# Optimization experiments

Measured on AMD Instinct MI355X. Metric: run time of the kernel, lower is better.

The kernel has to match this reference:

```python
import jax, jax.numpy as jnp
import numpy as np

NUM_EXPERTS = 8
HIDDEN = 2048
FFN = 1376
CAPACITY_FACTOR = 1.25
SCORE_SCALE = 1.0


def setup_inputs() -> dict:
    key = jax.random.key(0)
    k = jax.random.split(key, 6)
    T = 8192
    x = jax.random.normal(k[0], (T, HIDDEN), dtype=jnp.float32)
    topK_indices = jax.random.randint(k[1], (T,), 0, NUM_EXPERTS, dtype=jnp.int64)
    topK_scores = jax.random.uniform(k[2], (T,), dtype=jnp.float32)
    s = 1.0 / np.sqrt(HIDDEN)
    w_gate = jax.random.normal(k[3], (NUM_EXPERTS, HIDDEN, FFN), dtype=jnp.float32) * s
    w_up = jax.random.normal(k[4], (NUM_EXPERTS, HIDDEN, FFN), dtype=jnp.float32) * s
    w_down = jax.random.normal(k[5], (NUM_EXPERTS, FFN, HIDDEN), dtype=jnp.float32) * (1.0 / np.sqrt(FFN))
    return {"x": x, "topK_indices": topK_indices, "topK_scores": topK_scores,
            "w_gate": w_gate, "w_up": w_up, "w_down": w_down}


def reference(x, topK_indices, topK_scores, w_gate, w_up, w_down):
    T, D = x.shape
    E = w_gate.shape[0]
    capacity = int(CAPACITY_FACTOR * T / E)  # static (depends only on shapes)
    # position of each token within its assigned expert (deterministic drop:
    # keep the first `capacity` tokens in sequence order per expert)
    oh = jax.nn.one_hot(topK_indices, E, dtype=jnp.int32)          # [T,E]
    rank = jnp.take_along_axis(jnp.cumsum(oh, axis=0) - 1,
                               topK_indices[:, None].astype(jnp.int32), axis=1)[:, 0]
    keep = rank < capacity                                          # [T]
    # dispatch into per-expert capacity buffers; dropped tokens go to dummy slot
    slot = jnp.where(keep, topK_indices.astype(jnp.int32) * capacity + rank, E * capacity)
    buf = jnp.zeros((E * capacity + 1, D), x.dtype)
    buf = buf.at[slot].set(jnp.where(keep[:, None], x, jnp.zeros_like(x)))
    xe = buf[:E * capacity].reshape(E, capacity, D)                 # [E,C,D]
    # per-expert SwiGLU MLP as grouped GEMMs
    h = jax.nn.silu(jnp.einsum('ecd,edf->ecf', xe, w_gate)) * jnp.einsum('ecd,edf->ecf', xe, w_up)
    out = jnp.einsum('ecf,efd->ecd', h, w_down).reshape(E * capacity, D)
    out = jnp.concatenate([out, jnp.zeros((1, D), out.dtype)], axis=0)
    # combine: dropped tokens -> zero (dropped_padding='zero'), gate-score fusion
    y = out[slot] * keep[:, None].astype(out.dtype)
    y = y * (topK_scores[:, None] * SCORE_SCALE)
    return y
```

## Files before the change

kernel.cpp:

```cpp
#include <hip/hip_runtime.h>
#include <hip/hip_bf16.h>
#include <cstdint>
#include <cstddef>

#define NTOK 8192
#define DH   2048
#define DF   1376
#define NE   8
#define CAP  1280

typedef __bf16 bf16x8 __attribute__((ext_vector_type(8)));
typedef float  f32x4  __attribute__((ext_vector_type(4)));

#define BARRIER() asm volatile("s_barrier" ::: "memory")
#define WAITV(n)  asm volatile("s_waitcnt vmcnt(" #n ")" ::: "memory")
#define LGKM(n)   asm volatile("s_waitcnt lgkmcnt(" #n ")" ::: "memory")
#define SCHED0()  __builtin_amdgcn_sched_barrier(0)
#define SETPRIO(n) __builtin_amdgcn_s_setprio(n)

__device__ __forceinline__ uint32_t pk2(float a, float b) {
  float2 f; f.x = a; f.y = b;
  union { __hip_bfloat162 h; uint32_t u; } cv;
  cv.h = __float22bfloat162_rn(f);
  return cv.u;
}
__device__ __forceinline__ ushort bf16bits(float a) {
  return (ushort)(pk2(a, 0.f) & 0xFFFFu);
}
__device__ __forceinline__ void gload16(const ushort* g, ushort* l) {
  __builtin_amdgcn_global_load_lds(
      (const __attribute__((address_space(1))) uint32_t*)(const void*)g,
      (__attribute__((address_space(3))) uint32_t*)(void*)l,
      16, 0, 0);
}

__device__ __forceinline__ int rp_off(int row, int l4) {
  return ((row >> 1) << 7) + (((((row & 1) << 2) + l4) ^ ((row >> 1) & 7)) << 4);
}

__global__ void routing_kernel(const int* __restrict__ idx, int* __restrict__ tok_slot,
                               int* __restrict__ tok2slot) {
  __shared__ int cnt[256][NE];
  const int t = threadIdx.x;
  for (int s = t; s < NE * CAP; s += 256) tok_slot[s] = -1;
  unsigned long long cA = 0ull, cB = 0ull;
  const int per = NTOK / 256, base = t * per;
  for (int i = 0; i < per; ++i) {
    int e = idx[base + i];
    unsigned long long inc = 1ull << ((e & 3) * 16);
    if (e < 4) cA += inc; else cB += inc;
  }
#pragma unroll
  for (int e = 0; e < 4; ++e) cnt[t][e]     = (int)((cA >> (e * 16)) & 0xFFFF);
#pragma unroll
  for (int e = 0; e < 4; ++e) cnt[t][4 + e] = (int)((cB >> (e * 16)) & 0xFFFF);
  __syncthreads();
  if (t < NE) {
    int run = 0;
    for (int i = 0; i < 256; ++i) { int c = cnt[i][t]; cnt[i][t] = run; run += c; }
  }
  __syncthreads();
  cA = 0ull; cB = 0ull;
#pragma unroll
  for (int e = 0; e < 4; ++e) cA |= (unsigned long long)(cnt[t][e] & 0xFFFF) << (e * 16);
#pragma unroll
  for (int e = 0; e < 4; ++e) cB |= (unsigned long long)(cnt[t][4 + e] & 0xFFFF) << (e * 16);
  for (int i = 0; i < per; ++i) {
    int token = base + i;
    int e = idx[token];
    int sh = (e & 3) * 16;
    int r = (int)(((e < 4 ? cA : cB) >> sh) & 0xFFFF);
    unsigned long long inc = 1ull << sh;
    if (e < 4) cA += inc; else cB += inc;
    bool keep = (r < CAP);
    tok2slot[token] = keep ? (e * CAP + r) : -1;
    if (keep) tok_slot[e * CAP + r] = token;
  }
}

__global__ __launch_bounds__(256) void prep1(
    const float* __restrict__ wg, const float* __restrict__ wu,
    ushort* __restrict__ wgt, ushort* __restrict__ wut,
    const float* __restrict__ x, const int* __restrict__ tok2slot,
    ushort* __restrict__ xb2, float* __restrict__ y) {
  const int z = blockIdx.z;
  const int tid = threadIdx.x;
  if (z >= 16) {
    const int row = (z - 16) * 1024 + blockIdx.y * 32 + blockIdx.x;
    const int k0 = tid * 8;
    const size_t off = (size_t)row * DH + k0;
    float4 a = *(const float4*)(x + off);
    float4 b = *(const float4*)(x + off + 4);
    uint4 p4 = { pk2(a.x, a.y), pk2(a.z, a.w), pk2(b.x, b.y), pk2(b.z, b.w) };
    int slotg = tok2slot[row];
    if (slotg < 0) {
      float4 zz = {0.f, 0.f, 0.f, 0.f};
      *(float4*)(y + off) = zz;
      *(float4*)(y + off + 4) = zz;
    } else {
      int e = slotg / CAP, srow = slotg - e * CAP;
      int mt = srow >> 8, r = srow & 255;
      int kt = k0 >> 5, kk = k0 & 31;
      int p = r >> 1, g = ((r & 1) << 2) + (kk >> 3);
      size_t ou = (size_t)((e * 5 + mt) * 64 + kt) * 8192 + p * 64 + ((g ^ (p & 7)) << 3);
      *(uint4*)(xb2 + ou) = p4;
    }
    return;
  }
  const float* in; ushort* out; int eidx;
  if (z < 8) { in = wg; out = wgt; eidx = z; }
  else       { in = wu; out = wut; eidx = z - 8; }
  const int K = DH, N = DF;
  const int n0 = blockIdx.x * 64, k0 = blockIdx.y * 64;
  if (n0 >= N) return;
  __shared__ ushort T[64][72];
  const size_t eoff_in = (size_t)eidx * K * N;
  const int kr = tid >> 4;
  const int nc = (tid & 15) * 4;
#pragma unroll
  for (int it = 0; it < 4; ++it) {
    int k = k0 + kr + it * 16;
    int n = n0 + nc;
    float4 v = {0.f, 0.f, 0.f, 0.f};
    if (k < K && n + 4 <= N) v = *(const float4*)(in + eoff_in + (size_t)k * N + n);
    T[nc + 0][kr + it * 16] = bf16bits(v.x);
    T[nc + 1][kr + it * 16] = bf16bits(v.y);
    T[nc + 2][kr + it * 16] = bf16bits(v.z);
    T[nc + 3][kr + it * 16] = bf16bits(v.w);
  }
  __syncthreads();
  const int nr = tid >> 2;
  const int kc = tid & 3;
#pragma unroll
  for (int it = 0; it < 2; ++it) {
    int kloc = kc * 16 + it * 8;
    int n = n0 + nr, k = k0 + kloc;
    if (n < N && k + 8 <= K) {
      int nt = n >> 7, r = n & 127;
      int kt = k >> 5, kk = k & 31;
      int p = r >> 1, g = ((r & 1) << 2) + (kk >> 3);
      size_t ou = (size_t)((eidx * 11 + nt) * 64 + kt) * 4096 + p * 64 + ((g ^ (p & 7)) << 3);
      *(uint4*)(out + ou) = *(const uint4*)&T[nr][kloc];
    }
  }
}

__global__ __launch_bounds__(256) void prep_wd(
    const float* __restrict__ wd, ushort* __restrict__ wdt) {
  const int eidx = blockIdx.z;
  const int K = DF, N = DH;
  const int n0 = blockIdx.x * 64, k0 = blockIdx.y * 64;
  __shared__ ushort T[64][72];
  const int tid = threadIdx.x;
  const size_t eoff_in = (size_t)eidx * K * N;
  const int kr = tid >> 4;
  const int nc = (tid & 15) * 4;
#pragma unroll
  for (int it = 0; it < 4; ++it) {
    int k = k0 + kr + it * 16;
    int n = n0 + nc;
    float4 v = {0.f, 0.f, 0.f, 0.f};
    if (k < K && n + 4 <= N) v = *(const float4*)(wd + eoff_in + (size_t)k * N + n);
    T[nc + 0][kr + it * 16] = bf16bits(v.x);
    T[nc + 1][kr + it * 16] = bf16bits(v.y);
    T[nc + 2][kr + it * 16] = bf16bits(v.z);
    T[nc + 3][kr + it * 16] = bf16bits(v.w);
  }
  __syncthreads();
  const int nr = tid >> 2;
  const int kc = tid & 3;
#pragma unroll
  for (int it = 0; it < 2; ++it) {
    int kloc = kc * 16 + it * 8;
    int n = n0 + nr, k = k0 + kloc;
    if (n < N && k + 8 <= K) {
      int nt = n >> 7, r = n & 127;
      int kt = k >> 5, kk = k & 31;
      int p = r >> 1, g = ((r & 1) << 2) + (kk >> 3);
      size_t ou = (size_t)((eidx * 16 + nt) * 43 + kt) * 4096 + p * 64 + ((g ^ (p & 7)) << 3);
      *(uint4*)(wdt + ou) = *(const uint4*)&T[nr][kloc];
    }
  }
}

#define GU_READ(SET, RB) { \
  char* Ab_  = sm + (RB) * 16384; \
  char* Bgb_ = sm + 65536 + (RB) * 8192; \
  char* Bub_ = sm + 98304 + (RB) * 8192; \
  _Pragma("unroll") for (int i_ = 0; i_ < 4; ++i_) aR##SET[i_]  = *(const bf16x8*)(Ab_ + aoff[i_]); \
  _Pragma("unroll") for (int j_ = 0; j_ < 4; ++j_) bgR##SET[j_] = *(const bf16x8*)(Bgb_ + boff[j_]); \
  _Pragma("unroll") for (int j_ = 0; j_ < 4; ++j_) buR##SET[j_] = *(const bf16x8*)(Bub_ + boff[j_]); \
}
#define GU_MFMA(SET) { \
  _Pragma("unroll") for (int j_ = 0; j_ < 4; ++j_) \
    _Pragma("unroll") for (int i_ = 0; i_ < 4; ++i_) \
      accG[i_][j_] = __builtin_amdgcn_mfma_f32_16x16x32_bf16(aR##SET[i_], bgR##SET[j_], accG[i_][j_], 0, 0, 0); \
  _Pragma("unroll") for (int j_ = 0; j_ < 4; ++j_) \
    _Pragma("unroll") for (int i_ = 0; i_ < 4; ++i_) \
      accU[i_][j_] = __builtin_amdgcn_mfma_f32_16x16x32_bf16(aR##SET[i_], buR##SET[j_], accU[i_][j_], 0, 0, 0); \
}
#define GU_BODY(T, CUR, NXT) { \
  const int t_ = (T); \
  if (t_ + 3 < NT) { \
    const int w_ = (t_ + 3) & 3; \
    gload16(srcA[0] + (size_t)(t_ + 3) * 8192, (ushort*)(sm + w_ * 16384 + dstw)); \
    gload16(srcA[1] + (size_t)(t_ + 3) * 8192, (ushort*)(sm + w_ * 16384 + 8192 + dstw)); \
    gload16(srcBg + (size_t)(t_ + 3) * 4096, (ushort*)(sm + 65536 + w_ * 8192 + dstw)); \
    gload16(srcBu + (size_t)(t_ + 3) * 4096, (ushort*)(sm + 98304 + w_ * 8192 + dstw)); \
  } \
  if (t_ + 1 < NT) { GU_READ(NXT, (t_ + 1) & 3); LGKM(12); } else { LGKM(0); } \
  SCHED0(); SETPRIO(1); \
  GU_MFMA(CUR); \
  SETPRIO(0); SCHED0(); \
  if (t_ + 3 < NT) { WAITV(4); } else if (t_ + 2 < NT) { WAITV(0); } \
  BARRIER(); \
}

__global__ __launch_bounds__(512, 2) void gemm_gateup3(
    const ushort* __restrict__ xb2, const ushort* __restrict__ wgt,
    const ushort* __restrict__ wut, ushort* __restrict__ h)
{
  __shared__ __align__(16) char sm[131072];
  const int tid = threadIdx.x, lane = tid & 63, wid = tid >> 6;
  const int wr = wid >> 1, wc = wid & 1;
  const int l15 = lane & 15, l4 = lane >> 4;

  int wgid = (blockIdx.x & 7) * 55 + (blockIdx.x >> 3);
  const int e = wgid / 55;
  const int rem = wgid - e * 55;
  const int mt = rem / 11, nt = rem - (rem / 11) * 11;
  const int n0 = nt * 128;

  const ushort* srcA[2]; const ushort* srcBg; const ushort* srcBu;
  {
    const size_t abase = (size_t)((e * 5 + mt) * 64) * 8192;
    const int lo = (wid * 1024 + lane * 16) >> 1;
    srcA[0] = xb2 + abase + lo;
    srcA[1] = xb2 + abase + 4096 + lo;
    const size_t bbase = (size_t)((e * 11 + nt) * 64) * 4096;
    srcBg = wgt + bbase + lo;
    srcBu = wut + bbase + lo;
  }
  int aoff[4], boff[4];
#pragma unroll
  for (int i = 0; i < 4; ++i) aoff[i] = rp_off(wr * 64 + i * 16 + l15, l4);
#pragma unroll
  for (int j = 0; j < 4; ++j) boff[j] = rp_off(wc * 64 + j * 16 + l15, l4);
  const int dstw = wid * 1024;

  f32x4 accG[4][4], accU[4][4];
#pragma unroll
  for (int i = 0; i < 4; ++i)
#pragma unroll
    for (int j = 0; j < 4; ++j) {
      accG[i][j] = (f32x4){0.f, 0.f, 0.f, 0.f};
      accU[i][j] = (f32x4){0.f, 0.f, 0.f, 0.f};
    }

  const int NT = DH / 32;
#pragma unroll
  for (int t0 = 0; t0 < 3; ++t0) {
    gload16(srcA[0] + (size_t)t0 * 8192, (ushort*)(sm + t0 * 16384 + dstw));
    gload16(srcA[1] + (size_t)t0 * 8192, (ushort*)(sm + t0 * 16384 + 8192 + dstw));
    gload16(srcBg + (size_t)t0 * 4096, (ushort*)(sm + 65536 + t0 * 8192 + dstw));
    gload16(srcBu + (size_t)t0 * 4096, (ushort*)(sm + 98304 + t0 * 8192 + dstw));
  }
  WAITV(4);
  BARRIER();

  bf16x8 aR0[4], bgR0[4], buR0[4], aR1[4], bgR1[4], buR1[4];
  GU_READ(0, 0);

  for (int t = 0; t < NT; t += 2) {
    GU_BODY(t, 0, 1);
    GU_BODY(t + 1, 1, 0);
  }

  const size_t hbase = (size_t)((e * 5 + mt) * 43) * 8192;
#pragma unroll
  for (int j = 0; j < 4; ++j) {
    int col = n0 + wc * 64 + j * 16 + l15;
    if (col < DF) {
      int kt = col >> 5, kk = col & 31;
      int gb = kk >> 3, ke = kk & 7;
      const size_t cb = hbase + (size_t)kt * 8192;
#pragma unroll
      for (int i = 0; i < 4; ++i)
#pragma unroll
        for (int r2 = 0; r2 < 4; ++r2) {
          int rowloc = wr * 64 + i * 16 + l4 * 4 + r2;
          int p = rowloc >> 1, g = ((rowloc & 1) << 2) + gb;
          float gv = accG[i][j][r2], uv = accU[i][j][r2];
          h[cb + p * 64 + ((g ^ (p & 7)) << 3) + ke] = bf16bits(gv / (1.f + __expf(-gv)) * uv);
        }
    }
  }
}

#define DN_READ(SET, RB) { \
  char* Ab_ = sm + (RB) * 16384; \
  char* Bb_ = sm + 65536 + (RB) * 8192; \
  _Pragma("unroll") for (int i_ = 0; i_ < 4; ++i_) aR##SET[i_] = *(const bf16x8*)(Ab_ + aoff[i_]); \
  _Pragma("unroll") for (int j_ = 0; j_ < 4; ++j_) bR##SET[j_] = *(const bf16x8*)(Bb_ + boff[j_]); \
}
#define DN_MFMA(SET) { \
  _Pragma("unroll") for (int j_ = 0; j_ < 4; ++j_) \
    _Pragma("unroll") for (int i_ = 0; i_ < 4; ++i_) \
      acc[i_][j_] = __builtin_amdgcn_mfma_f32_16x16x32_bf16(aR##SET[i_], bR##SET[j_], acc[i_][j_], 0, 0, 0); \
}
#define DN_BODY(T, CUR, NXT) { \
  const int t_ = (T); \
  if (t_ + 3 < NT) { \
    const int w_ = (t_ + 3) & 3; \
    gload16(srcA[0] + (size_t)(t_ + 3) * 8192, (ushort*)(sm + w_ * 16384 + dstw)); \
    gload16(srcA[1] + (size_t)(t_ + 3) * 8192, (ushort*)(sm + w_ * 16384 + 8192 + dstw)); \
    gload16(srcB + (size_t)(t_ + 3) * 4096, (ushort*)(sm + 65536 + w_ * 8192 + dstw)); \
  } \
  if (t_ + 1 < NT) { DN_READ(NXT, (t_ + 1) & 3); LGKM(8); } else { LGKM(0); } \
  SCHED0(); SETPRIO(1); \
  DN_MFMA(CUR); \
  SETPRIO(0); SCHED0(); \
  if (t_ + 3 < NT) { WAITV(3); } else if (t_ + 2 < NT) { WAITV(0); } \
  BARRIER(); \
}

__global__ __launch_bounds__(512, 2) void gemm_down3(
    const ushort* __restrict__ h, const ushort* __restrict__ wdt,
    const int* __restrict__ tok_slot, const float* __restrict__ scores,
    float* __restrict__ y)
{
  __shared__ __align__(16) char sm[100352];
  int* tokc = (int*)(sm + 98304);
  float* scc = (float*)(sm + 99328);
  const int tid = threadIdx.x, lane = tid & 63, wid = tid >> 6;
  const int wr = wid >> 1, wc = wid & 1;
  const int l15 = lane & 15, l4 = lane >> 4;

  int wgid = (blockIdx.x & 7) * 80 + (blockIdx.x >> 3);
  const int e = wgid / 80;
  const int rem = wgid - e * 80;
  const int mt = rem / 16, nt = rem & 15;
  const int n0 = nt * 128;

  if (tid < 256) {
    int tk = tok_slot[e * CAP + mt * 256 + tid];
    tokc[tid] = tk;
    scc[tid] = (tk >= 0) ? scores[tk] : 0.f;
  }
  __syncthreads();

  const ushort* srcA[2]; const ushort* srcB;
  {
    const size_t abase = (size_t)((e * 5 + mt) * 43) * 8192;
    const int lo = (wid * 1024 + lane * 16) >> 1;
    srcA[0] = h + abase + lo;
    srcA[1] = h + abase + 4096 + lo;
    srcB = wdt + (size_t)((e * 16 + nt) * 43) * 4096 + lo;
  }
  int aoff[4], boff[4];
#pragma unroll
  for (int i = 0; i < 4; ++i) aoff[i] = rp_off(wr * 64 + i * 16 + l15, l4);
#pragma unroll
  for (int j = 0; j < 4; ++j) boff[j] = rp_off(wc * 64 + j * 16 + l15, l4);
  const int dstw = wid * 1024;

  f32x4 acc[4][4];
#pragma unroll
  for (int i = 0; i < 4; ++i)
#pragma unroll
    for (int j = 0; j < 4; ++j) acc[i][j] = (f32x4){0.f, 0.f, 0.f, 0.f};

  const int NT = DF / 32;
#pragma unroll
  for (int t0 = 0; t0 < 3; ++t0) {
    gload16(srcA[0] + (size_t)t0 * 8192, (ushort*)(sm + t0 * 16384 + dstw));
    gload16(srcA[1] + (size_t)t0 * 8192, (ushort*)(sm + t0 * 16384 + 8192 + dstw));
    gload16(srcB + (size_t)t0 * 4096, (ushort*)(sm + 65536 + t0 * 8192 + dstw));
  }
  WAITV(3);
  BARRIER();

  bf16x8 aR0[4], bR0[4], aR1[4], bR1[4];
  DN_READ(0, 0);

  for (int t = 0; t < NT - 1; t += 2) {
    DN_BODY(t, 0, 1);
    DN_BODY(t + 1, 1, 0);
  }
  DN_BODY(NT - 1, 0, 1);

  int tkr[4][4]; float sr[4][4];
#pragma unroll
  for (int i = 0; i < 4; ++i)
#pragma unroll
    for (int r = 0; r < 4; ++r) {
      int rl = wr * 64 + i * 16 + l4 * 4 + r;
      tkr[i][r] = tokc[rl];
      sr[i][r]  = scc[rl];
    }
#pragma unroll
  for (int j = 0; j < 4; ++j) {
    int col = n0 + wc * 64 + j * 16 + l15;
#pragma unroll
    for (int i = 0; i < 4; ++i)
#pragma unroll
      for (int r = 0; r < 4; ++r)
        if (tkr[i][r] >= 0)
          y[(size_t)tkr[i][r] * DH + col] = acc[i][j][r] * sr[i][r];
  }
}

extern "C" void kernel_launch(void* const* d_in, const int* in_sizes, int n_in,
                              void* d_out, int out_size, void* d_ws, size_t ws_size,
                              hipStream_t stream) {
  const float* x   = (const float*)d_in[0];
  const int*   idx = (const int*)d_in[1];
  const float* sc  = (const float*)d_in[2];
  const float* wg  = (const float*)d_in[3];
  const float* wu  = (const float*)d_in[4];
  const float* wd  = (const float*)d_in[5];
  float* y = (float*)d_out;

  const size_t OFF_T2S = 40960;
  const size_t OFF_H   = OFF_T2S + 32768;
  const size_t SZ_H    = (size_t)NE * 5 * 43 * 16384;
  const size_t OFF_XB  = OFF_H + SZ_H;
  const size_t SZ_XB   = (size_t)NE * 5 * 64 * 16384;
  const size_t OFF_WGT = OFF_XB + SZ_XB;
  const size_t SZ_WG   = (size_t)NE * 11 * 64 * 8192;
  const size_t OFF_WUT = OFF_WGT + SZ_WG;

  int* tok_slot = (int*)d_ws;
  int* tok2slot = (int*)((char*)d_ws + OFF_T2S);
  ushort* hbuf = (ushort*)((char*)d_ws + OFF_H);
  ushort* xb2  = (ushort*)((char*)d_ws + OFF_XB);
  ushort* wgt  = (ushort*)((char*)d_ws + OFF_WGT);
  ushort* wut  = (ushort*)((char*)d_ws + OFF_WUT);
  ushort* wdt  = wgt;

  hipLaunchKernelGGL(routing_kernel, dim3(1), dim3(256), 0, stream, idx, tok_slot, tok2slot);
  hipLaunchKernelGGL(prep1, dim3(32, 32, 24), dim3(256), 0, stream,
                     wg, wu, wgt, wut, x, tok2slot, xb2, y);
  hipLaunchKernelGGL(gemm_gateup3, dim3(440), dim3(512), 0, stream,
                     xb2, wgt, wut, hbuf);
  hipLaunchKernelGGL(prep_wd, dim3(32, 22, 8), dim3(256), 0, stream, wd, wdt);
  hipLaunchKernelGGL(gemm_down3, dim3(640), dim3(512), 0, stream,
                     hbuf, wdt, tok_slot, sc, y);
}
```

Measured before the change: 315.4 us.

## Shrink down-GEMM pipeline to 3 LDS stages and raise occupancy target

The down-projection GEMM drops from four LDS buffers with prefetch distance three to three buffers with distance two, and from double-buffered register fragments to a single set loaded and fully waited each step. This cuts LDS use from about 98KB to about 74KB, and launch_bounds now asks for 4 blocks per SM instead of 2, aiming for more waves to hide latency. The cost is less prefetch depth and no overlap of LDS reads with MFMA inside a wave. Register pressure at the higher occupancy target may force spills.

```diff
diff --git a/kernel.cpp b/kernel.cpp
--- a/kernel.cpp
+++ b/kernel.cpp
@@ -297,41 +297,14 @@
   }
 }
 
-#define DN_READ(SET, RB) { \
-  char* Ab_ = sm + (RB) * 16384; \
-  char* Bb_ = sm + 65536 + (RB) * 8192; \
-  _Pragma("unroll") for (int i_ = 0; i_ < 4; ++i_) aR##SET[i_] = *(const bf16x8*)(Ab_ + aoff[i_]); \
-  _Pragma("unroll") for (int j_ = 0; j_ < 4; ++j_) bR##SET[j_] = *(const bf16x8*)(Bb_ + boff[j_]); \
-}
-#define DN_MFMA(SET) { \
-  _Pragma("unroll") for (int j_ = 0; j_ < 4; ++j_) \
-    _Pragma("unroll") for (int i_ = 0; i_ < 4; ++i_) \
-      acc[i_][j_] = __builtin_amdgcn_mfma_f32_16x16x32_bf16(aR##SET[i_], bR##SET[j_], acc[i_][j_], 0, 0, 0); \
-}
-#define DN_BODY(T, CUR, NXT) { \
-  const int t_ = (T); \
-  if (t_ + 3 < NT) { \
-    const int w_ = (t_ + 3) & 3; \
-    gload16(srcA[0] + (size_t)(t_ + 3) * 8192, (ushort*)(sm + w_ * 16384 + dstw)); \
-    gload16(srcA[1] + (size_t)(t_ + 3) * 8192, (ushort*)(sm + w_ * 16384 + 8192 + dstw)); \
-    gload16(srcB + (size_t)(t_ + 3) * 4096, (ushort*)(sm + 65536 + w_ * 8192 + dstw)); \
-  } \
-  if (t_ + 1 < NT) { DN_READ(NXT, (t_ + 1) & 3); LGKM(8); } else { LGKM(0); } \
-  SCHED0(); SETPRIO(1); \
-  DN_MFMA(CUR); \
-  SETPRIO(0); SCHED0(); \
-  if (t_ + 3 < NT) { WAITV(3); } else if (t_ + 2 < NT) { WAITV(0); } \
-  BARRIER(); \
-}
-
-__global__ __launch_bounds__(512, 2) void gemm_down3(
+__global__ __launch_bounds__(512, 4) void gemm_down4(
     const ushort* __restrict__ h, const ushort* __restrict__ wdt,
     const int* __restrict__ tok_slot, const float* __restrict__ scores,
     float* __restrict__ y)
 {
-  __shared__ __align__(16) char sm[100352];
-  int* tokc = (int*)(sm + 98304);
-  float* scc = (float*)(sm + 99328);
+  __shared__ __align__(16) char sm[75776];
+  int* tokc = (int*)(sm + 73728);
+  float* scc = (float*)(sm + 74752);
   const int tid = threadIdx.x, lane = tid & 63, wid = tid >> 6;
   const int wr = wid >> 1, wc = wid & 1;
   const int l15 = lane & 15, l4 = lane >> 4;
@@ -372,23 +345,41 @@
 
   const int NT = DF / 32;
 #pragma unroll
-  for (int t0 = 0; t0 < 3; ++t0) {
+  for (int t0 = 0; t0 < 2; ++t0) {
     gload16(srcA[0] + (size_t)t0 * 8192, (ushort*)(sm + t0 * 16384 + dstw));
     gload16(srcA[1] + (size_t)t0 * 8192, (ushort*)(sm + t0 * 16384 + 8192 + dstw));
-    gload16(srcB + (size_t)t0 * 4096, (ushort*)(sm + 65536 + t0 * 8192 + dstw));
+    gload16(srcB + (size_t)t0 * 4096, (ushort*)(sm + 49152 + t0 * 8192 + dstw));
   }
   WAITV(3);
   BARRIER();
 
-  bf16x8 aR0[4], bR0[4], aR1[4], bR1[4];
-  DN_READ(0, 0);
-
-  for (int t = 0; t < NT - 1; t += 2) {
-    DN_BODY(t, 0, 1);
-    DN_BODY(t + 1, 1, 0);
-  }
-  DN_BODY(NT - 1, 0, 1);
-
+  int rb = 0, wb = 2;
+  for (int t = 0; t < NT; ++t) {
+    char* Ab = sm + rb * 16384;
+    char* Bb = sm + 49152 + rb * 8192;
+    if (t + 2 < NT) {
+      gload16(srcA[0] + (size_t)(t + 2) * 8192, (ushort*)(sm + wb * 16384 + dstw));
+      gload16(srcA[1] + (size_t)(t + 2) * 8192, (ushort*)(sm + wb * 16384 + 8192 + dstw));
+      gload16(srcB + (size_t)(t + 2) * 4096, (ushort*)(sm + 49152 + wb * 8192 + dstw));
+    }
+    bf16x8 a[4], b[4];
+#pragma unroll
+    for (int i = 0; i < 4; ++i) a[i] = *(const bf16x8*)(Ab + aoff[i]);
+#pragma unroll
+    for (int j = 0; j < 4; ++j) b[j] = *(const bf16x8*)(Bb + boff[j]);
+    LGKM(0); SCHED0();
+    SETPRIO(1);
+#pragma unroll
+    for (int j = 0; j < 4; ++j)
+#pragma unroll
+      for (int i = 0; i < 4; ++i)
+        acc[i][j] = __builtin_amdgcn_mfma_f32_16x16x32_bf16(a[i], b[j], acc[i][j], 0, 0, 0);
+    SETPRIO(0); SCHED0();
+    if (t + 2 < NT) { WAITV(3); } else { WAITV(0); }
+    BARRIER();
+    rb = (rb == 2) ? 0 : rb + 1;
+    wb = (wb == 2) ? 0 : wb + 1;
+  }
   int tkr[4][4]; float sr[4][4];
 #pragma unroll
   for (int i = 0; i < 4; ++i)
@@ -444,6 +435,6 @@
   hipLaunchKernelGGL(gemm_gateup3, dim3(440), dim3(512), 0, stream,
                      xb2, wgt, wut, hbuf);
   hipLaunchKernelGGL(prep_wd, dim3(32, 22, 8), dim3(256), 0, stream, wd, wdt);
-  hipLaunchKernelGGL(gemm_down3, dim3(640), dim3(512), 0, stream,
+  hipLaunchKernelGGL(gemm_down4, dim3(640), dim3(512), 0, stream,
                      hbuf, wdt, tok_slot, sc, y);
 }
```

Measured after the change: 318.0 us. No clear change (+0.8%).
